# Performance work log

Measured on AMD Instinct MI355X. Metric: run time of the kernel, lower is better.

The kernel has to match this reference:

```python
import jax, jax.numpy as jnp
import numpy as np

B, S, D, Q = 2, 2048, 2048, 16
H = D // Q  # head dim = 128


def _precompute_mask(s):
    # additive causal mask: -1e9 strictly above the diagonal
    m = jnp.full((s, s), -1000000000.0, dtype=jnp.float32)
    return jnp.triu(m, k=1)


def _precompute_rope(head, s):
    # inv_freq over even indices 0,2,...,head-2
    inv_freq = 1.0 / (10000.0 ** (jnp.arange(0, head, 2, dtype=jnp.float32) / head))  # [H/2]
    freqs = jnp.arange(s, dtype=jnp.float32)[:, None] * inv_freq[None, :]  # [S, H/2]
    emb = jnp.concatenate([freqs, freqs], axis=-1)  # [S, H]
    return jnp.sin(emb), jnp.cos(emb)


def _rotate_half(x):
    x1, x2 = jnp.split(x, 2, axis=-1)
    return jnp.concatenate([-x2, x1], axis=-1)


def _apply_rope(x, sin, cos):
    # x: [B, Q, S, H]; sin/cos: [S, H] broadcast over batch & heads
    return x * cos + _rotate_half(x) * sin


def setup_inputs() -> dict:
    key = jax.random.key(0)
    kx, kq, kk, kv, ko = jax.random.split(key, 5)
    wscale = 1.0 / np.sqrt(D)
    x = jax.random.normal(kx, (B, S, D), dtype=jnp.float32)
    wq = jax.random.normal(kq, (D, D), dtype=jnp.float32) * wscale
    wk = jax.random.normal(kk, (D, D), dtype=jnp.float32) * wscale
    wv = jax.random.normal(kv, (D, D), dtype=jnp.float32) * wscale
    wo = jax.random.normal(ko, (D, D), dtype=jnp.float32) * wscale
    mask = _precompute_mask(S)
    sin, cos = _precompute_rope(H, S)
    return {"x": x, "wq": wq, "wk": wk, "wv": wv, "wo": wo,
            "mask": mask, "sin": sin, "cos": cos}


def reference(x, wq, wk, wv, wo, mask, sin, cos):
    b, s, d = x.shape
    # projections: [B,S,D] @ [D, Q*H] -> [B,S,Q,H] -> [B,Q,S,H]
    def proj(w):
        t = jnp.einsum('bsd,de->bse', x, w).reshape(b, s, Q, H)
        return t.transpose(0, 2, 1, 3)
    q, k, v = proj(wq), proj(wk), proj(wv)
    q = _apply_rope(q, sin, cos)
    k = _apply_rope(k, sin, cos) * (H ** -0.5)
    # scores [B,Q,S,Skv] + causal mask, softmax over kv
    a = jnp.einsum('bqsh,bqth->bqst', q, k) + mask
    a = jax.nn.softmax(a, axis=-1)
    y = jnp.einsum('bqst,bqth->bqsh', a, v)  # [B,Q,S,H]
    y = y.transpose(0, 2, 1, 3).reshape(b, s, Q * H)  # [B,S,D]
    return jnp.einsum('bsd,de->bse', y, wo)
```

## Files before the change

### kernel.cpp

```cpp
#include <hip/hip_runtime.h>

typedef unsigned short u16;
typedef unsigned int u32;
typedef __attribute__((ext_vector_type(8))) short bf16x8;
typedef __attribute__((ext_vector_type(4))) float f32x4;
typedef __bf16 bf16v8 __attribute__((ext_vector_type(8)));

__device__ __forceinline__ u16 f2bf(float x) {
  u32 u = __float_as_uint(x);
  u32 r = (u + 0x7FFFu + ((u >> 16) & 1u)) >> 16;
  return (u16)r;
}
__device__ __forceinline__ float bf2f(u16 x) { return __uint_as_float(((u32)x) << 16); }

__device__ __forceinline__ void mfma_bf16(f32x4& d, bf16x8 a, bf16x8 b) {
  d = __builtin_amdgcn_mfma_f32_16x16x32_bf16(
        __builtin_bit_cast(bf16v8, a), __builtin_bit_cast(bf16v8, b), d, 0, 0, 0);
}

__device__ __forceinline__ void gload16(const u16* g, u16* l) {
  __builtin_amdgcn_global_load_lds((const __attribute__((address_space(1))) u32*)g,
                                   (__attribute__((address_space(3))) u32*)l, 16, 0, 0);
}

__device__ __forceinline__ void store_c(u16* p, float v) { *p = f2bf(v); }
__device__ __forceinline__ void store_c(float* p, float v) { *p = v; }

__global__ void cvt4(const float* __restrict__ in, u16* __restrict__ out, int n4) {
  int i = blockIdx.x * 256 + threadIdx.x;
  if (i >= n4) return;
  float4 v = reinterpret_cast<const float4*>(in)[i];
  u32 lo = (u32)f2bf(v.x) | ((u32)f2bf(v.y) << 16);
  u32 hi = (u32)f2bf(v.z) | ((u32)f2bf(v.w) << 16);
  reinterpret_cast<uint2*>(out)[i] = make_uint2(lo, hi);
}

__global__ void wtrans3(const float* __restrict__ wq, const float* __restrict__ wk,
                        const float* __restrict__ wv,
                        u16* __restrict__ wqkt, u16* __restrict__ wvt) {
  const float* in; u16* out;
  switch (blockIdx.z) {
    case 0: in = wq; out = wqkt; break;
    case 1: in = wk; out = wqkt + (size_t)2048 * 2048; break;
    default: in = wv; out = wvt; break;
  }
  __shared__ float t[32][33];
  int n0 = blockIdx.x * 32, k0 = blockIdx.y * 32;
  int tx = threadIdx.x, ty = threadIdx.y;
#pragma unroll
  for (int j = 0; j < 4; ++j)
    t[ty + 8 * j][tx] = in[(size_t)(k0 + ty + 8 * j) * 2048 + n0 + tx];
  __syncthreads();
#pragma unroll
  for (int j = 0; j < 4; ++j)
    out[(size_t)(n0 + ty + 8 * j) * 2048 + k0 + tx] = f2bf(t[tx][ty + 8 * j]);
}

__global__ void wtrans1(const float* __restrict__ in, u16* __restrict__ out) {
  __shared__ float t[32][33];
  int n0 = blockIdx.x * 32, k0 = blockIdx.y * 32;
  int tx = threadIdx.x, ty = threadIdx.y;
#pragma unroll
  for (int j = 0; j < 4; ++j)
    t[ty + 8 * j][tx] = in[(size_t)(k0 + ty + 8 * j) * 2048 + n0 + tx];
  __syncthreads();
#pragma unroll
  for (int j = 0; j < 4; ++j)
    out[(size_t)(n0 + ty + 8 * j) * 2048 + k0 + tx] = f2bf(t[tx][ty + 8 * j]);
}

template <typename CT>
__global__ __launch_bounds__(256) void gemm_bt(const u16* __restrict__ A,
                                               const u16* __restrict__ Bt,
                                               CT* __restrict__ C,
                                               int M, int N, int K) {
  __shared__ u16 As[2][128 * 32];
  __shared__ u16 Bs[2][128 * 32];
  int tid = threadIdx.x;
  int lane = tid & 63, wave = tid >> 6;
  int g = lane >> 4, lr = lane & 15;
  int wr = wave >> 1, wc = wave & 1;
  size_t brow = (size_t)blockIdx.y * 128, bcol = (size_t)blockIdx.x * 128;

  auto stage = [&](int kt, int bf) {
#pragma unroll
    for (int i = 0; i < 2; ++i) {
      int c = i * 256 + tid;
      gload16(A + (brow + (c >> 2)) * (size_t)K + kt + (c & 3) * 8, &As[bf][c * 8]);
      gload16(Bt + (bcol + (c >> 2)) * (size_t)K + kt + (c & 3) * 8, &Bs[bf][c * 8]);
    }
  };

  f32x4 acc[4][4];
#pragma unroll
  for (int m = 0; m < 4; ++m)
#pragma unroll
    for (int n = 0; n < 4; ++n) acc[m][n] = (f32x4){0.f, 0.f, 0.f, 0.f};

  stage(0, 0);
  __syncthreads();
  int buf = 0;
  for (int kt = 0; kt < K; kt += 32, buf ^= 1) {
    if (kt + 32 < K) stage(kt + 32, buf ^ 1);
    bf16x8 af[4], bf[4];
#pragma unroll
    for (int m = 0; m < 4; ++m)
      af[m] = *(const bf16x8*)&As[buf][(wr * 64 + m * 16 + lr) * 32 + g * 8];
#pragma unroll
    for (int n = 0; n < 4; ++n)
      bf[n] = *(const bf16x8*)&Bs[buf][(wc * 64 + n * 16 + lr) * 32 + g * 8];
#pragma unroll
    for (int m = 0; m < 4; ++m)
#pragma unroll
      for (int n = 0; n < 4; ++n) mfma_bf16(acc[m][n], af[m], bf[n]);
    __syncthreads();
  }
#pragma unroll
  for (int m = 0; m < 4; ++m)
#pragma unroll
    for (int n = 0; n < 4; ++n) {
      size_t row = brow + wr * 64 + m * 16 + 4 * g;
      size_t col = bcol + wc * 64 + n * 16 + lr;
#pragma unroll
      for (int r = 0; r < 4; ++r) store_c(&C[(row + r) * (size_t)N + col], acc[m][n][r]);
    }
}

__global__ __launch_bounds__(512, 2) void gemm256(const u16* __restrict__ A,
                                                  const u16* __restrict__ Bt,
                                                  u16* __restrict__ C,
                                                  int M, int N, int K) {
  __shared__ u16 lds[2][16384];
  int tid = threadIdx.x;
  int lane = tid & 63, wave = tid >> 6;
  int g = lane >> 4, lr = lane & 15;
  int wr = wave >> 2, wc = wave & 3;
  size_t brow = (size_t)blockIdx.y * 256, bcol = (size_t)blockIdx.x * 256;

  auto stage = [&](int kt, int bf) {
#pragma unroll
    for (int i = 0; i < 4; ++i) {
      int c = i * 512 + tid;
      int part = c >> 10;
      int p = c & 1023;
      int row = p >> 2, pc = p & 3;
      int lc = pc ^ ((row >> 1) & 3);
      const u16* src = part == 0
          ? A  + (brow + row) * (size_t)K + kt + lc * 8
          : Bt + (bcol + row) * (size_t)K + kt + lc * 8;
      gload16(src, &lds[bf][part * 8192 + p * 8]);
    }
  };

  f32x4 acc[8][4];
#pragma unroll
  for (int m = 0; m < 8; ++m)
#pragma unroll
    for (int n = 0; n < 4; ++n) acc[m][n] = (f32x4){0.f, 0.f, 0.f, 0.f};

  int NT = K >> 5;
  stage(0, 0);
  stage(32, 1);
  for (int t = 0; t < NT; ++t) {
    if (t == NT - 1) asm volatile("s_waitcnt vmcnt(0)" ::: "memory");
    else             asm volatile("s_waitcnt vmcnt(4)" ::: "memory");
    __builtin_amdgcn_s_barrier();
    int bf = t & 1;
    const u16* La = &lds[bf][0];
    const u16* Lb = &lds[bf][8192];
    bf16x8 bfr[4];
#pragma unroll
    for (int n = 0; n < 4; ++n) {
      int colr = wc * 64 + n * 16 + lr;
      bfr[n] = *(const bf16x8*)&Lb[colr * 32 + ((g ^ ((colr >> 1) & 3)) * 8)];
    }
#pragma unroll
    for (int m = 0; m < 8; ++m) {
      int rowr = wr * 128 + m * 16 + lr;
      bf16x8 afr = *(const bf16x8*)&La[rowr * 32 + ((g ^ ((rowr >> 1) & 3)) * 8)];
#pragma unroll
      for (int n = 0; n < 4; ++n) mfma_bf16(acc[m][n], afr, bfr[n]);
    }
    __builtin_amdgcn_s_barrier();
    if (t + 2 < NT) stage((t + 2) * 32, bf);
  }
#pragma unroll
  for (int m = 0; m < 8; ++m)
#pragma unroll
    for (int n = 0; n < 4; ++n) {
      size_t row = brow + wr * 128 + m * 16 + 4 * g;
      size_t col = bcol + wc * 64 + n * 16 + lr;
#pragma unroll
      for (int r = 0; r < 4; ++r) C[(row + r) * (size_t)N + col] = f2bf(acc[m][n][r]);
    }
}

__global__ void rope_kernel(u16* __restrict__ qk,
                            const float* __restrict__ sn, const float* __restrict__ cs) {
  int idx = blockIdx.x * 256 + threadIdx.x;
  int d = idx & 63;
  int h = (idx >> 6) & 15;
  int bs = idx >> 10;
  int s = bs & 2047;
  size_t base = ((size_t)bs << 12) + h * 128;
  float c1 = cs[s * 128 + d], c2 = cs[s * 128 + d + 64];
  float s1 = sn[s * 128 + d], s2 = sn[s * 128 + d + 64];
  float q1 = bf2f(qk[base + d]), q2 = bf2f(qk[base + d + 64]);
  float k1 = bf2f(qk[base + 2048 + d]), k2 = bf2f(qk[base + 2048 + d + 64]);
  qk[base + d]      = f2bf(q1 * c1 - q2 * s1);
  qk[base + d + 64] = f2bf(q2 * c2 + q1 * s2);
  const float ks = 0.08838834764831845f;
  qk[base + 2048 + d]      = f2bf((k1 * c1 - k2 * s1) * ks);
  qk[base + 2048 + d + 64] = f2bf((k2 * c2 + k1 * s2) * ks);
}

__global__ __launch_bounds__(512, 2) void attn(const u16* __restrict__ qk,
                                               const u16* __restrict__ vt,
                                               u16* __restrict__ y) {
  __shared__ u16 Ks[3][64 * 128];
  __shared__ u16 Vs[3][128 * 64];
  __shared__ u32 P_lds[8][16][33];
  int tid = threadIdx.x;
  int wave = tid >> 6, lane = tid & 63;
  int g = lane >> 4, lr = lane & 15;
  int b = blockIdx.z, h = blockIdx.y, bx = blockIdx.x;

  const u16* Q  = qk + ((size_t)b * 2048) * 4096 + h * 128;
  const u16* K  = qk + ((size_t)b * 2048) * 4096 + 2048 + h * 128;
  const u16* Vg = vt + (size_t)h * 128 * 4096 + (size_t)b * 2048;
  u16* Y = y + ((size_t)b * 2048) * 2048 + h * 128;

  auto stage = [&](int kv0, int bf) {
#pragma unroll
    for (int i = 0; i < 2; ++i) {
      int c = tid + 512 * i;
      int krow = c >> 4, kphys = (c & 15) << 4;
      gload16(K + (size_t)(kv0 + krow) * 4096 + ((kphys ^ ((krow & 7) << 4)) >> 1),
              &Ks[bf][c * 8]);
      int vrow = c >> 3, vphys = c & 7;
      gload16(Vg + (size_t)vrow * 4096 + kv0 + ((vphys ^ (vrow & 7)) * 8),
              &Vs[bf][c * 8]);
    }
  };

  for (int seg = 0; seg < 2; ++seg) {
    int sup = seg ? (15 - bx) : bx;
    int ntiles = 2 * sup + 2;
    int q0w = sup * 128 + wave * 16;

    bf16x8 qfr[4];
#pragma unroll
    for (int dc = 0; dc < 4; ++dc)
      qfr[dc] = *(const bf16x8*)&Q[(size_t)(q0w + lr) * 4096 + dc * 32 + g * 8];

    f32x4 o[8];
#pragma unroll
    for (int i = 0; i < 8; ++i) o[i] = (f32x4){0.f, 0.f, 0.f, 0.f};
    float lsum = 0.f;

    __syncthreads();
    stage(0, 0);
    stage(64, 1);
    if (ntiles > 2) stage(128, 2);
    int buf = 0;
    for (int t = 0; t < ntiles; ++t) {
      int w = ntiles - 1 - t;
      if (w >= 2)      asm volatile("s_waitcnt vmcnt(8)" ::: "memory");
      else if (w == 1) asm volatile("s_waitcnt vmcnt(4)" ::: "memory");
      else             asm volatile("s_waitcnt vmcnt(0)" ::: "memory");
      __builtin_amdgcn_s_barrier();
      int kv0 = t * 64;
      f32x4 st[4];
#pragma unroll
      for (int n = 0; n < 4; ++n) {
        f32x4 s4 = (f32x4){0.f, 0.f, 0.f, 0.f};
        int row = n * 16 + lr;
#pragma unroll
        for (int dc = 0; dc < 4; ++dc) {
          bf16x8 kfr = *(const bf16x8*)
              &Ks[buf][row * 128 + (((dc * 64 + 16 * g) ^ ((row & 7) << 4)) >> 1)];
          mfma_bf16(s4, kfr, qfr[dc]);
        }
        st[n] = s4;
      }
      int qg = q0w + lr;
      u32 pk[8];
#pragma unroll
      for (int n = 0; n < 4; ++n)
#pragma unroll
        for (int rp = 0; rp < 2; ++rp) {
          int kvb = kv0 + n * 16 + 4 * g + rp * 2;
          float p0 = (kvb     <= qg) ? __expf(st[n][rp * 2])     : 0.f;
          float p1 = (kvb + 1 <= qg) ? __expf(st[n][rp * 2 + 1]) : 0.f;
          lsum += p0 + p1;
          pk[n * 2 + rp] = (u32)f2bf(p0) | ((u32)f2bf(p1) << 16);
        }
#pragma unroll
      for (int n = 0; n < 4; ++n) {
        P_lds[wave][lr][8 * n + 2 * g]     = pk[n * 2];
        P_lds[wave][lr][8 * n + 2 * g + 1] = pk[n * 2 + 1];
      }
      asm volatile("" ::: "memory");
#pragma unroll
      for (int kh = 0; kh < 2; ++kh) {
        union { u32 w[4]; bf16x8 v; } pu;
#pragma unroll
        for (int j = 0; j < 4; ++j)
          pu.w[j] = P_lds[wave][lr][16 * kh + 4 * g + j];
        bf16x8 pf = pu.v;
#pragma unroll
        for (int dch = 0; dch < 8; ++dch) {
          int vr = dch * 16 + lr;
          bf16x8 vfr = *(const bf16x8*)
              &Vs[buf][vr * 64 + (((4 * kh + g) ^ (lr & 7)) * 8)];
          mfma_bf16(o[dch], pf, vfr);
        }
      }
      __builtin_amdgcn_s_barrier();
      if (t + 3 < ntiles) stage((t + 3) * 64, buf);
      buf = (buf == 2) ? 0 : buf + 1;
    }
    lsum += __shfl_xor(lsum, 16);
    lsum += __shfl_xor(lsum, 32);
    float linv[4];
#pragma unroll
    for (int r = 0; r < 4; ++r) linv[r] = 1.f / __shfl(lsum, 4 * g + r);
#pragma unroll
    for (int dch = 0; dch < 8; ++dch)
#pragma unroll
      for (int r = 0; r < 4; ++r)
        Y[(size_t)(q0w + 4 * g + r) * 2048 + dch * 16 + lr] = f2bf(o[dch][r] * linv[r]);
  }
}

extern "C" void kernel_launch(void* const* d_in, const int* in_sizes, int n_in,
                              void* d_out, int out_size, void* d_ws, size_t ws_size,
                              hipStream_t stream) {
  const float* x  = (const float*)d_in[0];
  const float* wq = (const float*)d_in[1];
  const float* wk = (const float*)d_in[2];
  const float* wv = (const float*)d_in[3];
  const float* wo = (const float*)d_in[4];
  const float* sn = (const float*)d_in[6];
  const float* cs = (const float*)d_in[7];

  char* W = (char*)d_ws;
  u16* xb   = (u16*)(W);
  u16* wqkt = (u16*)(W + (size_t)16 * 1024 * 1024);
  u16* wvt  = (u16*)(W + (size_t)32 * 1024 * 1024);
  u16* vt   = (u16*)(W + (size_t)40 * 1024 * 1024);
  u16* qkb  = (u16*)d_out;
  u16* yb   = xb;

  dim3 tb(32, 8);
  cvt4<<<8192, 256, 0, stream>>>(x, xb, 2097152);
  wtrans3<<<dim3(64, 64, 3), tb, 0, stream>>>(wq, wk, wv, wqkt, wvt);
  gemm256<<<dim3(16, 16), 512, 0, stream>>>(xb, wqkt, qkb, 4096, 4096, 2048);
  gemm_bt<u16><<<dim3(32, 16), 256, 0, stream>>>(wvt, xb, vt, 2048, 4096, 2048);
  wtrans1<<<dim3(64, 64), tb, 0, stream>>>(wo, wvt);
  rope_kernel<<<16384, 256, 0, stream>>>(qkb, sn, cs);
  attn<<<dim3(8, 16, 2), 512, 0, stream>>>(qkb, vt, yb);
  gemm_bt<float><<<dim3(16, 32), 256, 0, stream>>>(yb, wvt, (float*)d_out, 4096, 2048, 2048);
}
```

Before: 279.4 us.

## Generalize swizzled 256-tile GEMM and use it for V and output projections

Replaces the simple 128x128 double-buffered gemm_bt with a templated version of the swizzled, vmcnt-pipelined gemm256 kernel. The V projection now uses 256x128 tiles and the output projection uses 128x256 tiles, both with 512 threads. This raises per-block data reuse and brings LDS bank-conflict swizzling and async prefetch to those GEMMs. s_setprio is also added around the MFMA section. The trade-off is fewer blocks (256 per GEMM) on a 256-CU part, which may leave some CUs underused.

```diff
diff --git a/kernel.cpp b/kernel.cpp
--- a/kernel.cpp
+++ b/kernel.cpp
@@ -69,129 +69,77 @@
     out[(size_t)(n0 + ty + 8 * j) * 2048 + k0 + tx] = f2bf(t[tx][ty + 8 * j]);
 }
 
-template <typename CT>
-__global__ __launch_bounds__(256) void gemm_bt(const u16* __restrict__ A,
-                                               const u16* __restrict__ Bt,
-                                               CT* __restrict__ C,
-                                               int M, int N, int K) {
-  __shared__ u16 As[2][128 * 32];
-  __shared__ u16 Bs[2][128 * 32];
+template <int BM, int BN, int WM, int WN, typename CT>
+__global__ __launch_bounds__(512, 2) void gemm256t(const u16* __restrict__ A,
+                                                   const u16* __restrict__ Bt,
+                                                   CT* __restrict__ C,
+                                                   int M, int N, int K) {
+  constexpr int MR = BM / WM / 16;
+  constexpr int NR = BN / WN / 16;
+  constexpr int CH = (BM + BN) / 128;
+  __shared__ u16 lds[2][(BM + BN) * 32];
   int tid = threadIdx.x;
   int lane = tid & 63, wave = tid >> 6;
   int g = lane >> 4, lr = lane & 15;
-  int wr = wave >> 1, wc = wave & 1;
-  size_t brow = (size_t)blockIdx.y * 128, bcol = (size_t)blockIdx.x * 128;
+  int wr = wave / WN, wc = wave % WN;
+  size_t brow = (size_t)blockIdx.y * BM, bcol = (size_t)blockIdx.x * BN;
 
   auto stage = [&](int kt, int bf) {
 #pragma unroll
-    for (int i = 0; i < 2; ++i) {
-      int c = i * 256 + tid;
-      gload16(A + (brow + (c >> 2)) * (size_t)K + kt + (c & 3) * 8, &As[bf][c * 8]);
-      gload16(Bt + (bcol + (c >> 2)) * (size_t)K + kt + (c & 3) * 8, &Bs[bf][c * 8]);
-    }
-  };
-
-  f32x4 acc[4][4];
-#pragma unroll
-  for (int m = 0; m < 4; ++m)
-#pragma unroll
-    for (int n = 0; n < 4; ++n) acc[m][n] = (f32x4){0.f, 0.f, 0.f, 0.f};
-
-  stage(0, 0);
-  __syncthreads();
-  int buf = 0;
-  for (int kt = 0; kt < K; kt += 32, buf ^= 1) {
-    if (kt + 32 < K) stage(kt + 32, buf ^ 1);
-    bf16x8 af[4], bf[4];
-#pragma unroll
-    for (int m = 0; m < 4; ++m)
-      af[m] = *(const bf16x8*)&As[buf][(wr * 64 + m * 16 + lr) * 32 + g * 8];
-#pragma unroll
-    for (int n = 0; n < 4; ++n)
-      bf[n] = *(const bf16x8*)&Bs[buf][(wc * 64 + n * 16 + lr) * 32 + g * 8];
-#pragma unroll
-    for (int m = 0; m < 4; ++m)
-#pragma unroll
-      for (int n = 0; n < 4; ++n) mfma_bf16(acc[m][n], af[m], bf[n]);
-    __syncthreads();
-  }
-#pragma unroll
-  for (int m = 0; m < 4; ++m)
-#pragma unroll
-    for (int n = 0; n < 4; ++n) {
-      size_t row = brow + wr * 64 + m * 16 + 4 * g;
-      size_t col = bcol + wc * 64 + n * 16 + lr;
-#pragma unroll
-      for (int r = 0; r < 4; ++r) store_c(&C[(row + r) * (size_t)N + col], acc[m][n][r]);
-    }
-}
-
-__global__ __launch_bounds__(512, 2) void gemm256(const u16* __restrict__ A,
-                                                  const u16* __restrict__ Bt,
-                                                  u16* __restrict__ C,
-                                                  int M, int N, int K) {
-  __shared__ u16 lds[2][16384];
-  int tid = threadIdx.x;
-  int lane = tid & 63, wave = tid >> 6;
-  int g = lane >> 4, lr = lane & 15;
-  int wr = wave >> 2, wc = wave & 3;
-  size_t brow = (size_t)blockIdx.y * 256, bcol = (size_t)blockIdx.x * 256;
-
-  auto stage = [&](int kt, int bf) {
-#pragma unroll
-    for (int i = 0; i < 4; ++i) {
+    for (int i = 0; i < CH; ++i) {
       int c = i * 512 + tid;
-      int part = c >> 10;
-      int p = c & 1023;
+      bool isA = c < BM * 4;
+      int p = isA ? c : c - BM * 4;
       int row = p >> 2, pc = p & 3;
       int lc = pc ^ ((row >> 1) & 3);
-      const u16* src = part == 0
-          ? A  + (brow + row) * (size_t)K + kt + lc * 8
-          : Bt + (bcol + row) * (size_t)K + kt + lc * 8;
-      gload16(src, &lds[bf][part * 8192 + p * 8]);
+      const u16* src = isA ? A  + (brow + row) * (size_t)K + kt + lc * 8
+                           : Bt + (bcol + row) * (size_t)K + kt + lc * 8;
+      gload16(src, &lds[bf][(isA ? 0 : BM * 32) + p * 8]);
     }
   };
 
-  f32x4 acc[8][4];
-#pragma unroll
-  for (int m = 0; m < 8; ++m)
-#pragma unroll
-    for (int n = 0; n < 4; ++n) acc[m][n] = (f32x4){0.f, 0.f, 0.f, 0.f};
+  f32x4 acc[MR][NR];
+#pragma unroll
+  for (int m = 0; m < MR; ++m)
+#pragma unroll
+    for (int n = 0; n < NR; ++n) acc[m][n] = (f32x4){0.f, 0.f, 0.f, 0.f};
 
   int NT = K >> 5;
   stage(0, 0);
   stage(32, 1);
   for (int t = 0; t < NT; ++t) {
     if (t == NT - 1) asm volatile("s_waitcnt vmcnt(0)" ::: "memory");
-    else             asm volatile("s_waitcnt vmcnt(4)" ::: "memory");
+    else             asm volatile("s_waitcnt vmcnt(%0)" :: "i"(CH) : "memory");
     __builtin_amdgcn_s_barrier();
     int bf = t & 1;
     const u16* La = &lds[bf][0];
-    const u16* Lb = &lds[bf][8192];
-    bf16x8 bfr[4];
-#pragma unroll
-    for (int n = 0; n < 4; ++n) {
-      int colr = wc * 64 + n * 16 + lr;
+    const u16* Lb = &lds[bf][BM * 32];
+    __builtin_amdgcn_s_setprio(1);
+    bf16x8 bfr[NR];
+#pragma unroll
+    for (int n = 0; n < NR; ++n) {
+      int colr = wc * (BN / WN) + n * 16 + lr;
       bfr[n] = *(const bf16x8*)&Lb[colr * 32 + ((g ^ ((colr >> 1) & 3)) * 8)];
     }
 #pragma unroll
-    for (int m = 0; m < 8; ++m) {
-      int rowr = wr * 128 + m * 16 + lr;
+    for (int m = 0; m < MR; ++m) {
+      int rowr = wr * (BM / WM) + m * 16 + lr;
       bf16x8 afr = *(const bf16x8*)&La[rowr * 32 + ((g ^ ((rowr >> 1) & 3)) * 8)];
 #pragma unroll
-      for (int n = 0; n < 4; ++n) mfma_bf16(acc[m][n], afr, bfr[n]);
-    }
+      for (int n = 0; n < NR; ++n) mfma_bf16(acc[m][n], afr, bfr[n]);
+    }
+    __builtin_amdgcn_s_setprio(0);
     __builtin_amdgcn_s_barrier();
     if (t + 2 < NT) stage((t + 2) * 32, bf);
   }
 #pragma unroll
-  for (int m = 0; m < 8; ++m)
-#pragma unroll
-    for (int n = 0; n < 4; ++n) {
-      size_t row = brow + wr * 128 + m * 16 + 4 * g;
-      size_t col = bcol + wc * 64 + n * 16 + lr;
-#pragma unroll
-      for (int r = 0; r < 4; ++r) C[(row + r) * (size_t)N + col] = f2bf(acc[m][n][r]);
+  for (int m = 0; m < MR; ++m)
+#pragma unroll
+    for (int n = 0; n < NR; ++n) {
+      size_t row = brow + wr * (BM / WM) + m * 16 + 4 * g;
+      size_t col = bcol + wc * (BN / WN) + n * 16 + lr;
+#pragma unroll
+      for (int r = 0; r < 4; ++r) store_c(&C[(row + r) * (size_t)N + col], acc[m][n][r]);
     }
 }
 
@@ -355,10 +303,13 @@
   dim3 tb(32, 8);
   cvt4<<<8192, 256, 0, stream>>>(x, xb, 2097152);
   wtrans3<<<dim3(64, 64, 3), tb, 0, stream>>>(wq, wk, wv, wqkt, wvt);
-  gemm256<<<dim3(16, 16), 512, 0, stream>>>(xb, wqkt, qkb, 4096, 4096, 2048);
-  gemm_bt<u16><<<dim3(32, 16), 256, 0, stream>>>(wvt, xb, vt, 2048, 4096, 2048);
+  gemm256t<256, 256, 2, 4, u16><<<dim3(16, 16), 512, 0, stream>>>(
+      xb, wqkt, qkb, 4096, 4096, 2048);
+  gemm256t<256, 128, 4, 2, u16><<<dim3(32, 8), 512, 0, stream>>>(
+      wvt, xb, vt, 2048, 4096, 2048);
   wtrans1<<<dim3(64, 64), tb, 0, stream>>>(wo, wvt);
   rope_kernel<<<16384, 256, 0, stream>>>(qkb, sn, cs);
   attn<<<dim3(8, 16, 2), 512, 0, stream>>>(qkb, vt, yb);
-  gemm_bt<float><<<dim3(16, 32), 256, 0, stream>>>(yb, wvt, (float*)d_out, 4096, 2048, 2048);
-}
+  gemm256t<128, 256, 2, 4, float><<<dim3(8, 32), 512, 0, stream>>>(
+      yb, wvt, (float*)d_out, 4096, 2048, 2048);
+}
```

New measurement: 274.5 us. No clear change (-1.8%).
